# Kernel tuning notes

Measured on AMD Instinct MI355X. Metric: run time of the kernel, lower is better.

The kernel has to match this reference:

```python
import jax, jax.numpy as jnp
import numpy as np

N = 256
M = 180


def _fft3_centered(u):
    # centered 3D FFT: shift so that frequency 0 is at index n//2
    return jnp.fft.fftshift(jnp.fft.fftn(jnp.fft.ifftshift(u)))


def _ifft2_centered(s):
    ax = (-2, -1)
    return jnp.fft.fftshift(jnp.fft.ifft2(jnp.fft.ifftshift(s, axes=ax), axes=ax), axes=ax)


def _trilinear(F, pos):
    """Sample complex 3D grid F (n,n,n) at fractional index positions pos (...,3).
    Points outside the grid contribute zero (frequencies beyond Nyquist)."""
    n = F.shape[0]
    p0f = jnp.floor(pos)
    f = pos - p0f                      # fractional part, in [0,1)
    p0 = p0f.astype(jnp.int32)
    acc = jnp.zeros(pos.shape[:-1], dtype=F.dtype)
    for dx in (0, 1):
        for dy in (0, 1):
            for dz in (0, 1):
                idx = p0 + jnp.array([dx, dy, dz], jnp.int32)
                w = ((f[..., 0] if dx else 1.0 - f[..., 0])
                     * (f[..., 1] if dy else 1.0 - f[..., 1])
                     * (f[..., 2] if dz else 1.0 - f[..., 2]))
                valid = jnp.all((idx >= 0) & (idx < n), axis=-1)
                idc = jnp.clip(idx, 0, n - 1)
                val = F[idc[..., 0], idc[..., 1], idc[..., 2]]  # irregular gather
                acc = acc + jnp.where(valid, w, 0.0) * val
    return acc


def _lamino_fwd(weight, theta, tilt):
    """NUFFT laminography forward projector (Fourier-slice formulation).
    weight: (n,n,n,2) real/imag volume; theta: (M,) angles; tilt: scalar.
    Returns (M,n,n,2) projections, matching tike's Lamino.fwd math: the 2D
    Fourier transform of each projection equals the 3D FT of the volume
    sampled on a plane tilted by `tilt` and rotated by `theta` about z."""
    n = weight.shape[0]
    u = jax.lax.complex(weight[..., 0], weight[..., 1])
    F = _fft3_centered(u)                                   # (n,n,n) complex64
    fr = ((jnp.arange(n) - n // 2) / n).astype(jnp.float32)  # [-0.5, 0.5)
    kv, ku = jnp.meshgrid(fr, fr, indexing='ij')            # detector freq grid
    ct, st = jnp.cos(theta), jnp.sin(theta)                 # (M,)
    cp_, sp = jnp.cos(tilt), jnp.sin(tilt)
    one = jnp.ones_like(ct)
    e_u = jnp.stack([ct, st, 0.0 * ct], -1)                 # (M,3) horizontal axis
    e_v = jnp.stack([-st * cp_, ct * cp_, sp * one], -1)    # (M,3) tilted axis
    # 3D non-uniform frequencies for every (angle, detector pixel): (M,n,n,3)
    k3 = ku[None, :, :, None] * e_u[:, None, None, :] + kv[None, :, :, None] * e_v[:, None, None, :]
    pos = k3 * n + n // 2                                   # fractional grid coords
    samples = _trilinear(F, pos)                            # (M,n,n) complex
    proj = _ifft2_centered(samples)                         # (M,n,n) complex
    return jnp.stack([proj.real, proj.imag], -1).astype(jnp.float32)


def setup_inputs() -> dict:
    key = jax.random.key(0)
    k1, k2 = jax.random.split(key)
    weight = jax.random.normal(k1, (N, N, N, 2), dtype=jnp.float32)
    theta = jax.random.uniform(k2, (M,), dtype=jnp.float32) * (2.0 * np.pi)
    tilt = jnp.float32(1.0)  # laminography tilt angle (rad); source default pi/2
    return {"weight": weight, "theta": theta, "tilt": tilt}


def reference(weight, theta, tilt):
    return _lamino_fwd(weight, theta, tilt)
```

## Files before the change

### kernel.cpp

```cpp
#include <hip/hip_runtime.h>
#include <math.h>


namespace {

template<int MODE, bool INV>
__global__ __launch_bounds__(256)
void fft_pass(const float2* in, float2* out) {
  __shared__ float sre[8][265];
  __shared__ float sim[8][265];
  __shared__ float twr[128];
  __shared__ float twi[128];
  const int t = threadIdx.x;
  if (t < 128) {
    const float TWO_PI = 6.28318530717958647692f;
    float ang = (INV ? TWO_PI : -TWO_PI) * ((float)t * (1.0f / 256.0f));
    float s, c;
    sincosf(ang, &s, &c);
    twr[t] = c;
    twi[t] = s;
  }
  int l, j0, base, stride;
  if (MODE == 0) { l = t >> 5; j0 = t & 31; }
  else           { l = t & 7;  j0 = t >> 3; }
  const int lineIdx = (int)blockIdx.x * 8 + l;
  if (MODE == 0)      { base = lineIdx * 256;                            stride = 1;     }
  else if (MODE == 1) { base = (lineIdx >> 8) * 65536 + (lineIdx & 255); stride = 256;   }
  else                { base = lineIdx;                                  stride = 65536; }

  #pragma unroll
  for (int r = 0; r < 8; r++) {
    int j = j0 + 32 * r;
    float2 v = in[base + j * stride];
    float sgn = (j & 1) ? -1.0f : 1.0f;
    sre[l][j] = v.x * sgn;
    sim[l][j] = v.y * sgn;
  }
  __syncthreads();

  const int line = t >> 5;
  const int lane = t & 31;
  #pragma unroll
  for (int s = 0; s < 8; s++) {
    const int half = 128 >> s;
    #pragma unroll
    for (int r = 0; r < 4; r++) {
      int b   = lane + 32 * r;
      int pos = b & (half - 1);
      int grp = b >> (7 - s);
      int i   = (grp << (8 - s)) + pos;
      int j   = i + half;
      float ar = sre[line][i], ai = sim[line][i];
      float br = sre[line][j], bi = sim[line][j];
      sre[line][i] = ar + br;
      sim[line][i] = ai + bi;
      float dr = ar - br, di = ai - bi;
      int mm = pos << s;
      float wr = twr[mm], wi = twi[mm];
      sre[line][j] = dr * wr - di * wi;
      sim[line][j] = dr * wi + di * wr;
    }
    __syncthreads();
  }

  const float scale = INV ? (1.0f / 256.0f) : 1.0f;
  #pragma unroll
  for (int r = 0; r < 8; r++) {
    int j = j0 + 32 * r;
    int rev = (int)(__brev((unsigned)j) >> 24);
    float sgn = (j & 1) ? -scale : scale;
    float2 v;
    v.x = sre[l][rev] * sgn;
    v.y = sim[l][rev] * sgn;
    out[base + j * stride] = v;
  }
}

__global__ __launch_bounds__(256)
void sample_kernel(const float2* __restrict__ F, float2* __restrict__ out,
                   const float* __restrict__ theta, const float* __restrict__ tiltp) {
  __shared__ float2 tile[16][18];
  const int m  = blockIdx.z;
  const int tx = threadIdx.x;
  const int ty = threadIdx.y;
  const int a = blockIdx.x * 16 + tx;
  const int b = blockIdx.y * 16 + ty;
  float th = theta[m];
  float st, ct;
  sincosf(th, &st, &ct);
  float tl = tiltp[0];
  float sp, cp;
  sincosf(tl, &sp, &cp);
  float bu = (float)(b - 128);
  float av = (float)(a - 128);
  float p0 = bu * ct + av * (-st * cp) + 128.0f;
  float p1 = bu * st + av * (ct * cp) + 128.0f;
  float p2 = av * sp + 128.0f;
  float f0 = floorf(p0), f1 = floorf(p1), f2 = floorf(p2);
  int x0 = (int)f0, y0 = (int)f1, z0 = (int)f2;
  float fx = p0 - f0, fy = p1 - f1, fz = p2 - f2;
  float accr = 0.0f, acci = 0.0f;
  #pragma unroll
  for (int dx = 0; dx < 2; dx++) {
    int x = x0 + dx;
    bool vx = (x >= 0) && (x < 256);
    int xc = min(max(x, 0), 255);
    float wx = dx ? fx : (1.0f - fx);
    #pragma unroll
    for (int dy = 0; dy < 2; dy++) {
      int y = y0 + dy;
      bool vy = vx && (y >= 0) && (y < 256);
      int yc = min(max(y, 0), 255);
      float wxy = wx * (dy ? fy : (1.0f - fy));
      int rowbase = (xc * 256 + yc) * 256;
      #pragma unroll
      for (int dz = 0; dz < 2; dz++) {
        int z = z0 + dz;
        bool v = vy && (z >= 0) && (z < 256);
        int zc = min(max(z, 0), 255);
        float w = v ? wxy * (dz ? fz : (1.0f - fz)) : 0.0f;
        float2 c = F[rowbase + zc];
        accr += w * c.x;
        acci += w * c.y;
      }
    }
  }
  tile[ty][tx] = make_float2(accr, acci);
  __syncthreads();
  const int oa = blockIdx.x * 16 + ty;
  const int ob = blockIdx.y * 16 + tx;
  out[((size_t)m * 256 + oa) * 256 + ob] = tile[tx][ty];
}

}

extern "C" void kernel_launch(void* const* d_in, const int* in_sizes, int n_in,
                              void* d_out, int out_size, void* d_ws, size_t ws_size,
                              hipStream_t stream) {
  const float2* w  = (const float2*)d_in[0];
  const float*  th = (const float*)d_in[1];
  const float*  tl = (const float*)d_in[2];
  float2* F    = (float2*)d_ws;
  float2* out2 = (float2*)d_out;

  fft_pass<0, false><<<8192, 256, 0, stream>>>(w, F);
  fft_pass<1, false><<<8192, 256, 0, stream>>>(F, F);
  fft_pass<2, false><<<8192, 256, 0, stream>>>(F, F);

  dim3 g(16, 16, 180), blk(16, 16);
  sample_kernel<<<g, blk, 0, stream>>>(F, out2, th, tl);

  fft_pass<0, true><<<5760, 256, 0, stream>>>(out2, out2);
  fft_pass<1, true><<<5760, 256, 0, stream>>>(out2, out2);
}
```

Baseline: 637.1 us.

## Replace shared-memory radix-2 FFT with register-based 16x16 four-step FFT

Rewrites each 256-point FFT pass as a four-step decomposition: two register-resident 16-point FFTs joined by a single padded shared-memory transpose with inline twiddle recurrence. This removes the eight barrier-separated shared-memory butterfly stages and the twiddle table setup. Each block now processes 16 lines, so launch grids are halved. It increases register pressure and relies on a recurrence for twiddles, which may add small rounding error.

```diff
diff --git a/kernel.cpp b/kernel.cpp
--- a/kernel.cpp
+++ b/kernel.cpp
@@ -4,75 +4,95 @@
 
 namespace {
 
+__device__ __forceinline__ void fft16_reg(float (&re)[16], float (&im)[16],
+                                          bool inv) {
+  const float C16[8] = {1.0f, 0.92387953251128675613f, 0.70710678118654752440f,
+                        0.38268343236508977173f, 0.0f, -0.38268343236508977173f,
+                        -0.70710678118654752440f, -0.92387953251128675613f};
+  const float S16[8] = {0.0f, 0.38268343236508977173f, 0.70710678118654752440f,
+                        0.92387953251128675613f, 1.0f, 0.92387953251128675613f,
+                        0.70710678118654752440f, 0.38268343236508977173f};
+  #pragma unroll
+  for (int s = 0; s < 4; s++) {
+    const int h = 8 >> s;
+    #pragma unroll
+    for (int g = 0; g < (8 >> (3 - s)); g++) {
+      #pragma unroll
+      for (int p = 0; p < h; p++) {
+        const int i = g * 2 * h + p;
+        const int j = i + h;
+        const float ar = re[i], ai = im[i], br = re[j], bi = im[j];
+        re[i] = ar + br;
+        im[i] = ai + bi;
+        const float dr = ar - br, di = ai - bi;
+        const int t = p << s;
+        const float wr = C16[t];
+        const float wi = inv ? S16[t] : -S16[t];
+        re[j] = dr * wr - di * wi;
+        im[j] = dr * wi + di * wr;
+      }
+    }
+  }
+}
+
 template<int MODE, bool INV>
 __global__ __launch_bounds__(256)
-void fft_pass(const float2* in, float2* out) {
-  __shared__ float sre[8][265];
-  __shared__ float sim[8][265];
-  __shared__ float twr[128];
-  __shared__ float twi[128];
-  const int t = threadIdx.x;
-  if (t < 128) {
-    const float TWO_PI = 6.28318530717958647692f;
-    float ang = (INV ? TWO_PI : -TWO_PI) * ((float)t * (1.0f / 256.0f));
-    float s, c;
-    sincosf(ang, &s, &c);
-    twr[t] = c;
-    twi[t] = s;
-  }
-  int l, j0, base, stride;
-  if (MODE == 0) { l = t >> 5; j0 = t & 31; }
-  else           { l = t & 7;  j0 = t >> 3; }
-  const int lineIdx = (int)blockIdx.x * 8 + l;
+void fft_pass(const float2* __restrict__ in, float2* __restrict__ out) {
+  __shared__ float2 zt[16 * 273];
+  const int t  = threadIdx.x;
+  const int tx = t & 15;
+  const int ty = t >> 4;
+  const int idA = (MODE == 0) ? tx : ty;
+  const int lin = (MODE == 0) ? ty : tx;
+  const int lineIdx = (int)blockIdx.x * 16 + lin;
+  int base, stride;
   if (MODE == 0)      { base = lineIdx * 256;                            stride = 1;     }
   else if (MODE == 1) { base = (lineIdx >> 8) * 65536 + (lineIdx & 255); stride = 256;   }
   else                { base = lineIdx;                                  stride = 65536; }
 
-  #pragma unroll
-  for (int r = 0; r < 8; r++) {
-    int j = j0 + 32 * r;
-    float2 v = in[base + j * stride];
-    float sgn = (j & 1) ? -1.0f : 1.0f;
-    sre[l][j] = v.x * sgn;
-    sim[l][j] = v.y * sgn;
+  const int BR4[16] = {0, 8, 4, 12, 2, 10, 6, 14, 1, 9, 5, 13, 3, 11, 7, 15};
+
+  float re[16], im[16];
+
+  {
+    const float s1 = (idA & 1) ? -1.0f : 1.0f;
+    #pragma unroll
+    for (int n2 = 0; n2 < 16; n2++) {
+      const float2 v = in[base + (idA + 16 * n2) * stride];
+      re[n2] = v.x * s1;
+      im[n2] = v.y * s1;
+    }
+    fft16_reg(re, im, INV);
+    const float TWO_PI = 6.28318530717958647692f;
+    const float ang = (INV ? TWO_PI : -TWO_PI) * ((float)idA * (1.0f / 256.0f));
+    float ss, cc;
+    sincosf(ang, &ss, &cc);
+    float wr = 1.0f, wi = 0.0f;
+    #pragma unroll
+    for (int k2 = 0; k2 < 16; k2++) {
+      const float yr = re[BR4[k2]], yi = im[BR4[k2]];
+      zt[lin * 273 + idA * 17 + k2] =
+          make_float2(yr * wr - yi * wi, yr * wi + yi * wr);
+      const float nwr = wr * cc - wi * ss;
+      wi = wr * ss + wi * cc;
+      wr = nwr;
+    }
   }
   __syncthreads();
-
-  const int line = t >> 5;
-  const int lane = t & 31;
-  #pragma unroll
-  for (int s = 0; s < 8; s++) {
-    const int half = 128 >> s;
+  {
     #pragma unroll
-    for (int r = 0; r < 4; r++) {
-      int b   = lane + 32 * r;
-      int pos = b & (half - 1);
-      int grp = b >> (7 - s);
-      int i   = (grp << (8 - s)) + pos;
-      int j   = i + half;
-      float ar = sre[line][i], ai = sim[line][i];
-      float br = sre[line][j], bi = sim[line][j];
-      sre[line][i] = ar + br;
-      sim[line][i] = ai + bi;
-      float dr = ar - br, di = ai - bi;
-      int mm = pos << s;
-      float wr = twr[mm], wi = twi[mm];
-      sre[line][j] = dr * wr - di * wi;
-      sim[line][j] = dr * wi + di * wr;
+    for (int n1 = 0; n1 < 16; n1++) {
+      const float2 z = zt[lin * 273 + n1 * 17 + idA];
+      re[n1] = z.x;
+      im[n1] = z.y;
     }
-    __syncthreads();
-  }
-
-  const float scale = INV ? (1.0f / 256.0f) : 1.0f;
-  #pragma unroll
-  for (int r = 0; r < 8; r++) {
-    int j = j0 + 32 * r;
-    int rev = (int)(__brev((unsigned)j) >> 24);
-    float sgn = (j & 1) ? -scale : scale;
-    float2 v;
-    v.x = sre[l][rev] * sgn;
-    v.y = sim[l][rev] * sgn;
-    out[base + j * stride] = v;
+    fft16_reg(re, im, INV);
+    const float sOut = ((idA & 1) ? -1.0f : 1.0f) * (INV ? (1.0f / 256.0f) : 1.0f);
+    #pragma unroll
+    for (int k1 = 0; k1 < 16; k1++) {
+      out[base + (idA + 16 * k1) * stride] =
+          make_float2(re[BR4[k1]] * sOut, im[BR4[k1]] * sOut);
+    }
   }
 }
 
@@ -143,13 +163,13 @@
   float2* F    = (float2*)d_ws;
   float2* out2 = (float2*)d_out;
 
-  fft_pass<0, false><<<8192, 256, 0, stream>>>(w, F);
-  fft_pass<1, false><<<8192, 256, 0, stream>>>(F, F);
-  fft_pass<2, false><<<8192, 256, 0, stream>>>(F, F);
+  fft_pass<0, false><<<4096, 256, 0, stream>>>(w, F);
+  fft_pass<1, false><<<4096, 256, 0, stream>>>(F, F);
+  fft_pass<2, false><<<4096, 256, 0, stream>>>(F, F);
 
   dim3 g(16, 16, 180), blk(16, 16);
   sample_kernel<<<g, blk, 0, stream>>>(F, out2, th, tl);
 
-  fft_pass<0, true><<<5760, 256, 0, stream>>>(out2, out2);
-  fft_pass<1, true><<<5760, 256, 0, stream>>>(out2, out2);
+  fft_pass<0, true><<<2880, 256, 0, stream>>>(out2, out2);
+  fft_pass<1, true><<<2880, 256, 0, stream>>>(out2, out2);
 }
```

Measured after the change: 523.4 us. 1.22x faster.
